# Kernel optimization log

Measured on AMD Instinct MI355X. Metric: run time of the kernel, lower is better.

The kernel has to match this reference:

```python
import jax, jax.numpy as jnp
import numpy as np

N_NODES = 100000
IN_CH = 128
HID = 128   # 2 * out_channels
OUT = 64    # out_channels
N_EDGES = 1000000


def _glorot(key, shape):
    lim = np.sqrt(6.0 / (shape[0] + shape[1]))
    return jax.random.uniform(key, shape, jnp.float32, -lim, lim)


def setup_inputs() -> dict:
    key = jax.random.key(0)
    ks = jax.random.split(key, 8)
    x = jax.random.normal(ks[0], (N_NODES, IN_CH), jnp.float32)
    edge_index = jax.random.randint(ks[1], (2, N_EDGES), 0, N_NODES, jnp.int64)
    return {
        "x": x,
        "edge_index": edge_index,
        # conv1: in -> 2*out
        "W1_l": _glorot(ks[2], (IN_CH, HID)),
        "W1_r": _glorot(ks[3], (IN_CH, HID)),
        "b1": jnp.zeros((HID,), jnp.float32),
        # conv_mu: 2*out -> out
        "Wmu_l": _glorot(ks[4], (HID, OUT)),
        "Wmu_r": _glorot(ks[5], (HID, OUT)),
        "bmu": jnp.zeros((OUT,), jnp.float32),
        # conv_logstd: 2*out -> out
        "Wls_l": _glorot(ks[6], (HID, OUT)),
        "Wls_r": _glorot(ks[7], (HID, OUT)),
        "bls": jnp.zeros((OUT,), jnp.float32),
    }


def _sage_conv(x, src, dst, W_l, W_r, b, n_nodes):
    # mean-aggregate neighbor features: messages flow src -> dst (PyG source_to_target)
    agg = jax.ops.segment_sum(x[src], dst, num_segments=n_nodes)          # [N, d]
    deg = jax.ops.segment_sum(jnp.ones(src.shape, x.dtype), dst, num_segments=n_nodes)
    agg = agg / jnp.maximum(deg, 1.0)[:, None]
    return agg @ W_l + x @ W_r + b


def reference(x, edge_index, W1_l, W1_r, b1, Wmu_l, Wmu_r, bmu, Wls_l, Wls_r, bls):
    src, dst = edge_index[0], edge_index[1]
    n = x.shape[0]
    h = jax.nn.relu(_sage_conv(x, src, dst, W1_l, W1_r, b1, n))
    mu = _sage_conv(h, src, dst, Wmu_l, Wmu_r, bmu, n)
    logstd = _sage_conv(h, src, dst, Wls_l, Wls_r, bls, n)
    return (mu, logstd)
```

## Files before the change

### kernel.cpp

```cpp
#include <hip/hip_runtime.h>

#define NN 100000
#define IC 128
#define OC 64
#define NE 1000000

#define NBUCK 64
#define BN 1568
#define RCAP 18432
#define EPB 2048
#define CAPA 64
#define GPAD 16
#define LDW 136

typedef __attribute__((ext_vector_type(8))) short short8;
typedef __attribute__((ext_vector_type(4))) float f32x4;

static __device__ __forceinline__ float b2f(unsigned short u) {
    unsigned v = ((unsigned)u) << 16;
    float f;
    __builtin_memcpy(&f, &v, 4);
    return f;
}
static __device__ __forceinline__ unsigned short f2b(float f) {
    unsigned u;
    __builtin_memcpy(&u, &f, 4);
    u += 0x7fff + ((u >> 16) & 1);
    return (unsigned short)(u >> 16);
}

__global__ __launch_bounds__(256) void k_binA(const int* __restrict__ src,
                                              const int* __restrict__ dst,
                                              int* __restrict__ gcur,
                                              unsigned* __restrict__ bins) {
    __shared__ unsigned buf[NBUCK][CAPA];
    __shared__ int lcnt[NBUCK];
    const int t = threadIdx.x;
    if (t < NBUCK) lcnt[t] = 0;
    __syncthreads();
    const int e0 = blockIdx.x * EPB;
#pragma unroll
    for (int q = 0; q < EPB / 256; ++q) {
        int e = e0 + q * 256 + t;
        if (e < NE) {
            int d = dst[e];
            int s = src[e];
            int b = d / BN;
            unsigned packed = ((unsigned)(d - b * BN) << 17) | (unsigned)s;
            int idx = atomicAdd(&lcnt[b], 1);
            if (idx < CAPA) {
                buf[b][idx] = packed;
            } else {
                int g = atomicAdd(&gcur[b * GPAD], 1);
                if (g < RCAP) bins[(size_t)b * RCAP + g] = packed;
            }
        }
    }
    __syncthreads();
    const int wid = t >> 6, lane = t & 63;
    for (int b = wid * 16; b < wid * 16 + 16; ++b) {
        int c = lcnt[b];
        if (c > CAPA) c = CAPA;
        if (c > 0) {
            int g = 0;
            if (lane == 0) g = atomicAdd(&gcur[b * GPAD], c);
            g = __shfl(g, 0, 64);
            if (lane < c && g + lane < RCAP)
                bins[(size_t)b * RCAP + g + lane] = buf[b][lane];
        }
    }
}

__global__ __launch_bounds__(64) void k_bscan(const int* __restrict__ gcur,
                                              int* __restrict__ bstart,
                                              int* __restrict__ row_ptr) {
    const int t = threadIdx.x;
    int v = gcur[t * GPAD];
    if (v > RCAP) v = RCAP;
    int s = v;
    for (int off = 1; off < 64; off <<= 1) {
        int u = __shfl_up(s, off, 64);
        if (t >= off) s += u;
    }
    bstart[t] = s - v;
    if (t == 63) row_ptr[NN] = s;
}

__global__ __launch_bounds__(512) void k_binB(const int* __restrict__ gcur,
                                              const int* __restrict__ bstart,
                                              const unsigned* __restrict__ bins,
                                              int* __restrict__ row_ptr,
                                              int* __restrict__ csr) {
    __shared__ int lc[2048];
    __shared__ int rk[2048];
    __shared__ int tsum[512];
    __shared__ int seg[RCAP];
    const int b = blockIdx.x;
    const int t = threadIdx.x;
    const int base = b * BN;
    const int nloc = (NN - base < BN) ? (NN - base) : BN;
    for (int i = t; i < 2048; i += 512) { lc[i] = 0; rk[i] = 0; }
    __syncthreads();
    int c = gcur[b * GPAD];
    if (c > RCAP) c = RCAP;
    const unsigned* mb = bins + (size_t)b * RCAP;
    for (int i = t; i < c; i += 512) atomicAdd(&lc[mb[i] >> 17], 1);
    __syncthreads();
    int loc[4], s = 0;
#pragma unroll
    for (int q = 0; q < 4; ++q) { loc[q] = lc[t * 4 + q]; s += loc[q]; }
    tsum[t] = s;
    __syncthreads();
    for (int off = 1; off < 512; off <<= 1) {
        int u = (t >= off) ? tsum[t - off] : 0;
        __syncthreads();
        tsum[t] += u;
        __syncthreads();
    }
    int run = tsum[t] - s;
#pragma unroll
    for (int q = 0; q < 4; ++q) { lc[t * 4 + q] = run; run += loc[q]; }
    __syncthreads();
    const int bs = bstart[b];
    for (int i = t; i < nloc; i += 512) row_ptr[base + i] = bs + lc[i];
    for (int i = t; i < c; i += 512) {
        unsigned p = mb[i];
        int dl = p >> 17;
        int r = atomicAdd(&rk[dl], 1);
        seg[lc[dl] + r] = (int)(p & 0x1FFFFu);
    }
    __syncthreads();
    for (int i = t; i < c; i += 512) csr[bs + i] = seg[i];
}

__global__ __launch_bounds__(256) void k_cvt(const float* __restrict__ x,
                                             unsigned short* __restrict__ xb) {
    int t = blockIdx.x * 256 + threadIdx.x;
    if (t >= NN * IC / 8) return;
    const float4* p = (const float4*)x + (size_t)t * 2;
    float4 f0 = p[0], f1 = p[1];
    short8 o;
    o[0] = (short)f2b(f0.x); o[1] = (short)f2b(f0.y);
    o[2] = (short)f2b(f0.z); o[3] = (short)f2b(f0.w);
    o[4] = (short)f2b(f1.x); o[5] = (short)f2b(f1.y);
    o[6] = (short)f2b(f1.z); o[7] = (short)f2b(f1.w);
    *((short8*)xb + t) = o;
}

__global__ __launch_bounds__(256) void k_wprep(
    const float* __restrict__ W1l, const float* __restrict__ W1r,
    const float* __restrict__ Wml, const float* __restrict__ Wmr,
    const float* __restrict__ Wsl, const float* __restrict__ Wsr,
    unsigned short* __restrict__ Wf1, unsigned short* __restrict__ Wf2) {
    int t = blockIdx.x * 256 + threadIdx.x;
    if (t >= 2 * 4096) return;
    const int layer = t >> 12;
    const int f = t & 4095;
    const int lane = f & 63;
    const int nt = (f >> 6) & 7;
    const int ks = f >> 9;
    const int col = nt * 16 + (lane & 15);
    const int kb = ks * 32 + ((lane >> 4) << 3);
    short8 o;
#pragma unroll
    for (int e = 0; e < 8; ++e) {
        const int k = kb + e;
        float v;
        if (layer == 0) {
            v = (k < 128) ? W1l[k * 128 + col] : W1r[(k - 128) * 128 + col];
        } else {
            if (col < OC) v = (k < 128) ? Wml[k * OC + col] : Wmr[(k - 128) * OC + col];
            else {
                int c2 = col - OC;
                v = (k < 128) ? Wsl[k * OC + c2] : Wsr[(k - 128) * OC + c2];
            }
        }
        o[e] = (short)f2b(v);
    }
    unsigned short* W = (layer == 0) ? Wf1 : Wf2;
    *(short8*)(W + (size_t)f * 8) = o;
}

__global__ __launch_bounds__(256) void k_agg(const unsigned short* __restrict__ feat,
                                             const int* __restrict__ row_ptr,
                                             const int* __restrict__ csr,
                                             unsigned short* __restrict__ agg) {
    const int lane = threadIdx.x & 63;
    const int wid = threadIdx.x >> 6;
    const int slot = lane >> 4;
    const int cg = lane & 15;
    const int node = blockIdx.x * 16 + wid * 4 + slot;
    if (node >= NN) return;
    const int beg = row_ptr[node];
    const int end = row_ptr[node + 1];
    float acc[8];
#pragma unroll
    for (int q = 0; q < 8; ++q) acc[q] = 0.f;

    for (int j = beg; j < end; j += 8) {
        const int nl = end - j;
        short8 v[8];
#pragma unroll
        for (int u = 0; u < 8; ++u) {
            if (u < nl) {
                int s = csr[j + u];
                v[u] = *(const short8*)(feat + (size_t)s * IC + cg * 8);
            }
        }
#pragma unroll
        for (int u = 0; u < 8; ++u) {
            if (u < nl) {
#pragma unroll
                for (int q = 0; q < 8; ++q) acc[q] += b2f((unsigned short)v[u][q]);
            }
        }
    }
    float inv = 1.0f / fmaxf((float)(end - beg), 1.0f);
    short8 o;
#pragma unroll
    for (int q = 0; q < 8; ++q) o[q] = (short)f2b(acc[q] * inv);
    *(short8*)(agg + (size_t)node * IC + cg * 8) = o;
}

template <int MODE>
__global__ __launch_bounds__(256) void k_gemm(
    const unsigned short* __restrict__ Agg, const unsigned short* __restrict__ Xb,
    const unsigned short* __restrict__ Wf,
    const float* __restrict__ bias0, const float* __restrict__ bias1,
    unsigned short* __restrict__ hout, float* __restrict__ out_mu,
    float* __restrict__ out_ls) {
    const int lane = threadIdx.x & 63;
    const int wid = threadIdx.x >> 6;
    const int rowg = blockIdx.x * 128 + wid * 32;
    const int r16 = lane & 15;
    const int k8 = (lane >> 4) * 8;

    __shared__ short8 bsm[4096];

    int rA[2];
#pragma unroll
    for (int m = 0; m < 2; ++m) {
        int r = rowg + m * 16 + r16;
        rA[m] = (r < NN) ? r : (NN - 1);
    }

    short8 aF[2][8];
#pragma unroll
    for (int ks = 0; ks < 4; ++ks) {
        aF[0][ks] = *(const short8*)(Agg + (size_t)rA[0] * IC + ks * 32 + k8);
        aF[1][ks] = *(const short8*)(Agg + (size_t)rA[1] * IC + ks * 32 + k8);
    }
#pragma unroll
    for (int ks = 0; ks < 4; ++ks) {
        aF[0][4 + ks] = *(const short8*)(Xb + (size_t)rA[0] * IC + ks * 32 + k8);
        aF[1][4 + ks] = *(const short8*)(Xb + (size_t)rA[1] * IC + ks * 32 + k8);
    }

    const short8* Wg = (const short8*)Wf;
#pragma unroll
    for (int i = 0; i < 16; ++i)
        bsm[i * 256 + threadIdx.x] = Wg[i * 256 + threadIdx.x];

#pragma unroll
    for (int ks = 0; ks < 8; ++ks)
        asm volatile("" :: "v"(aF[0][ks]), "v"(aF[1][ks]));

    __syncthreads();

    f32x4 acc[2][8];
#pragma unroll
    for (int m = 0; m < 2; ++m)
#pragma unroll
        for (int nt = 0; nt < 8; ++nt) acc[m][nt] = (f32x4){0.f, 0.f, 0.f, 0.f};

#pragma unroll
    for (int ks = 0; ks < 8; ++ks) {
        short8 bF[8];
#pragma unroll
        for (int nt = 0; nt < 8; ++nt) bF[nt] = bsm[(ks * 8 + nt) * 64 + lane];
#pragma unroll
        for (int nt = 0; nt < 8; ++nt) {
            acc[0][nt] = __builtin_amdgcn_mfma_f32_16x16x32_bf16(aF[0][ks], bF[nt], acc[0][nt], 0, 0, 0);
            acc[1][nt] = __builtin_amdgcn_mfma_f32_16x16x32_bf16(aF[1][ks], bF[nt], acc[1][nt], 0, 0, 0);
        }
    }

    const int rbase = (lane >> 4) * 4;
    if (MODE == 0) {
        __syncthreads();
        unsigned short* ws = (unsigned short*)bsm + wid * 32 * LDW;
#pragma unroll
        for (int m = 0; m < 2; ++m) {
#pragma unroll
            for (int nt = 0; nt < 8; ++nt) {
                const int c = nt * 16 + r16;
                const float bv = bias0[c];
#pragma unroll
                for (int q = 0; q < 4; ++q) {
                    float v = fmaxf(acc[m][nt][q] + bv, 0.f);
                    ws[(m * 16 + rbase + q) * LDW + c] = f2b(v);
                }
            }
        }
        __syncthreads();
#pragma unroll
        for (int p = 0; p < 8; ++p) {
            const int rloc = p * 4 + (lane >> 4);
            const int row = rowg + rloc;
            if (row < NN) {
                short8 v = *(const short8*)&ws[rloc * LDW + r16 * 8];
                *(short8*)(hout + (size_t)row * IC + r16 * 8) = v;
            }
        }
    } else {
#pragma unroll
        for (int m = 0; m < 2; ++m) {
#pragma unroll
            for (int nt = 0; nt < 8; ++nt) {
                const int c = nt * 16 + r16;
                const float bv = (c < OC) ? bias0[c] : bias1[c - OC];
#pragma unroll
                for (int q = 0; q < 4; ++q) {
                    const int row = rowg + m * 16 + rbase + q;
                    if (row >= NN) continue;
                    float v = acc[m][nt][q] + bv;
                    if (c < OC) out_mu[(size_t)row * OC + c] = v;
                    else        out_ls[(size_t)row * OC + (c - OC)] = v;
                }
            }
        }
    }
}

extern "C" void kernel_launch(void* const* d_in, const int* in_sizes, int n_in,
                              void* d_out, int out_size, void* d_ws, size_t ws_size,
                              hipStream_t stream) {
    const float* x   = (const float*)d_in[0];
    const int*   ei  = (const int*)d_in[1];
    const float* W1l = (const float*)d_in[2];
    const float* W1r = (const float*)d_in[3];
    const float* b1  = (const float*)d_in[4];
    const float* Wml = (const float*)d_in[5];
    const float* Wmr = (const float*)d_in[6];
    const float* bm  = (const float*)d_in[7];
    const float* Wsl = (const float*)d_in[8];
    const float* Wsr = (const float*)d_in[9];
    const float* bs  = (const float*)d_in[10];

    const int* src = ei;
    const int* dst = ei + NE;

    char* w = (char*)d_ws;
    unsigned short* xb   = (unsigned short*)(w);
    unsigned short* hb   = (unsigned short*)(w + 25600000);
    unsigned short* aggb = (unsigned short*)(w + 51200000);
    unsigned short* Wf1  = (unsigned short*)(w + 76800000);
    unsigned short* Wf2  = (unsigned short*)(w + 76865536);
    int* row_ptr  = (int*)(w + 76931072);
    int* csr      = (int*)(w + 77331136);
    int* gcur     = (int*)(w + 81331136);
    int* bstart   = (int*)(w + 81335232);
    unsigned* bins = (unsigned*)(w + 81336256);

    float* out_mu = (float*)d_out;
    float* out_ls = out_mu + (size_t)NN * OC;

    const int gemm_grid = (NN + 127) / 128;
    const int agg_grid = (NN + 15) / 16;
    const int binA_grid = (NE + EPB - 1) / EPB;

    hipMemsetAsync(gcur, 0, NBUCK * GPAD * sizeof(int), stream);
    k_binA<<<binA_grid, 256, 0, stream>>>(src, dst, gcur, bins);
    k_bscan<<<1, 64, 0, stream>>>(gcur, bstart, row_ptr);
    k_binB<<<NBUCK, 512, 0, stream>>>(gcur, bstart, bins, row_ptr, csr);

    k_cvt<<<(NN * IC / 8 + 255) / 256, 256, 0, stream>>>(x, xb);
    k_wprep<<<(2 * 4096 + 255) / 256, 256, 0, stream>>>(W1l, W1r, Wml, Wmr, Wsl, Wsr, Wf1, Wf2);

    k_agg<<<agg_grid, 256, 0, stream>>>(xb, row_ptr, csr, aggb);
    k_gemm<0><<<gemm_grid, 256, 0, stream>>>(aggb, xb, Wf1, b1, nullptr,
                                             hb, nullptr, nullptr);

    k_agg<<<agg_grid, 256, 0, stream>>>(hb, row_ptr, csr, aggb);
    k_gemm<1><<<gemm_grid, 256, 0, stream>>>(aggb, hb, Wf2, bm, bs,
                                             nullptr, out_mu, out_ls);
}
```

Before: 200.4 us.

## Fold bucket scan into binB, merge prep kernels, halve GEMM weight LDS

Removes the separate single-block bucket-scan launch by having each binB block recompute the 64-entry prefix scan itself. Merges the x-to-bf16 conversion and weight-packing kernels into one launch. In the GEMM, weights are staged into shared memory in two halves (32 KB instead of 64 KB), with extra barriers between them, to raise occupancy. The cost is an added sync and a second weight load per block in exchange for fewer launches and more resident blocks.

```diff
diff --git a/kernel.cpp b/kernel.cpp
--- a/kernel.cpp
+++ b/kernel.cpp
@@ -12,6 +12,7 @@
 #define CAPA 64
 #define GPAD 16
 #define LDW 136
+#define CVT_BLOCKS 6250
 
 typedef __attribute__((ext_vector_type(8))) short short8;
 typedef __attribute__((ext_vector_type(4))) float f32x4;
@@ -71,23 +72,7 @@
     }
 }
 
-__global__ __launch_bounds__(64) void k_bscan(const int* __restrict__ gcur,
-                                              int* __restrict__ bstart,
-                                              int* __restrict__ row_ptr) {
-    const int t = threadIdx.x;
-    int v = gcur[t * GPAD];
-    if (v > RCAP) v = RCAP;
-    int s = v;
-    for (int off = 1; off < 64; off <<= 1) {
-        int u = __shfl_up(s, off, 64);
-        if (t >= off) s += u;
-    }
-    bstart[t] = s - v;
-    if (t == 63) row_ptr[NN] = s;
-}
-
 __global__ __launch_bounds__(512) void k_binB(const int* __restrict__ gcur,
-                                              const int* __restrict__ bstart,
                                               const unsigned* __restrict__ bins,
                                               int* __restrict__ row_ptr,
                                               int* __restrict__ csr) {
@@ -95,10 +80,22 @@
     __shared__ int rk[2048];
     __shared__ int tsum[512];
     __shared__ int seg[RCAP];
+    __shared__ int sh_bs;
     const int b = blockIdx.x;
     const int t = threadIdx.x;
     const int base = b * BN;
     const int nloc = (NN - base < BN) ? (NN - base) : BN;
+    if (t < 64) {
+        int v = gcur[t * GPAD];
+        if (v > RCAP) v = RCAP;
+        int s = v;
+        for (int off = 1; off < 64; off <<= 1) {
+            int u = __shfl_up(s, off, 64);
+            if (t >= off) s += u;
+        }
+        if (t == b) sh_bs = s - v;
+        if (b == 0 && t == 63) row_ptr[NN] = s;
+    }
     for (int i = t; i < 2048; i += 512) { lc[i] = 0; rk[i] = 0; }
     __syncthreads();
     int c = gcur[b * GPAD];
@@ -121,7 +118,7 @@
 #pragma unroll
     for (int q = 0; q < 4; ++q) { lc[t * 4 + q] = run; run += loc[q]; }
     __syncthreads();
-    const int bs = bstart[b];
+    const int bs = sh_bs;
     for (int i = t; i < nloc; i += 512) row_ptr[base + i] = bs + lc[i];
     for (int i = t; i < c; i += 512) {
         unsigned p = mb[i];
@@ -133,52 +130,52 @@
     for (int i = t; i < c; i += 512) csr[bs + i] = seg[i];
 }
 
-__global__ __launch_bounds__(256) void k_cvt(const float* __restrict__ x,
-                                             unsigned short* __restrict__ xb) {
-    int t = blockIdx.x * 256 + threadIdx.x;
-    if (t >= NN * IC / 8) return;
-    const float4* p = (const float4*)x + (size_t)t * 2;
-    float4 f0 = p[0], f1 = p[1];
-    short8 o;
-    o[0] = (short)f2b(f0.x); o[1] = (short)f2b(f0.y);
-    o[2] = (short)f2b(f0.z); o[3] = (short)f2b(f0.w);
-    o[4] = (short)f2b(f1.x); o[5] = (short)f2b(f1.y);
-    o[6] = (short)f2b(f1.z); o[7] = (short)f2b(f1.w);
-    *((short8*)xb + t) = o;
-}
-
-__global__ __launch_bounds__(256) void k_wprep(
+__global__ __launch_bounds__(256) void k_prep(
+    const float* __restrict__ x, unsigned short* __restrict__ xb,
     const float* __restrict__ W1l, const float* __restrict__ W1r,
     const float* __restrict__ Wml, const float* __restrict__ Wmr,
     const float* __restrict__ Wsl, const float* __restrict__ Wsr,
     unsigned short* __restrict__ Wf1, unsigned short* __restrict__ Wf2) {
-    int t = blockIdx.x * 256 + threadIdx.x;
-    if (t >= 2 * 4096) return;
-    const int layer = t >> 12;
-    const int f = t & 4095;
-    const int lane = f & 63;
-    const int nt = (f >> 6) & 7;
-    const int ks = f >> 9;
-    const int col = nt * 16 + (lane & 15);
-    const int kb = ks * 32 + ((lane >> 4) << 3);
-    short8 o;
-#pragma unroll
-    for (int e = 0; e < 8; ++e) {
-        const int k = kb + e;
-        float v;
-        if (layer == 0) {
-            v = (k < 128) ? W1l[k * 128 + col] : W1r[(k - 128) * 128 + col];
-        } else {
-            if (col < OC) v = (k < 128) ? Wml[k * OC + col] : Wmr[(k - 128) * OC + col];
-            else {
-                int c2 = col - OC;
-                v = (k < 128) ? Wsl[k * OC + c2] : Wsr[(k - 128) * OC + c2];
-            }
-        }
-        o[e] = (short)f2b(v);
-    }
-    unsigned short* W = (layer == 0) ? Wf1 : Wf2;
-    *(short8*)(W + (size_t)f * 8) = o;
+    const int blk = blockIdx.x;
+    if (blk < CVT_BLOCKS) {
+        int t = blk * 256 + threadIdx.x;
+        const float4* p = (const float4*)x + (size_t)t * 2;
+        float4 f0 = p[0], f1 = p[1];
+        short8 o;
+        o[0] = (short)f2b(f0.x); o[1] = (short)f2b(f0.y);
+        o[2] = (short)f2b(f0.z); o[3] = (short)f2b(f0.w);
+        o[4] = (short)f2b(f1.x); o[5] = (short)f2b(f1.y);
+        o[6] = (short)f2b(f1.z); o[7] = (short)f2b(f1.w);
+        *((short8*)xb + t) = o;
+    } else {
+        int t = (blk - CVT_BLOCKS) * 256 + threadIdx.x;
+        if (t >= 2 * 4096) return;
+        const int layer = t >> 12;
+        const int f = t & 4095;
+        const int lane = f & 63;
+        const int nt = (f >> 6) & 7;
+        const int ks = f >> 9;
+        const int col = nt * 16 + (lane & 15);
+        const int kb = ks * 32 + ((lane >> 4) << 3);
+        short8 o;
+#pragma unroll
+        for (int e = 0; e < 8; ++e) {
+            const int k = kb + e;
+            float v;
+            if (layer == 0) {
+                v = (k < 128) ? W1l[k * 128 + col] : W1r[(k - 128) * 128 + col];
+            } else {
+                if (col < OC) v = (k < 128) ? Wml[k * OC + col] : Wmr[(k - 128) * OC + col];
+                else {
+                    int c2 = col - OC;
+                    v = (k < 128) ? Wsl[k * OC + c2] : Wsr[(k - 128) * OC + c2];
+                }
+            }
+            o[e] = (short)f2b(v);
+        }
+        unsigned short* W = (layer == 0) ? Wf1 : Wf2;
+        *(short8*)(W + (size_t)f * 8) = o;
+    }
 }
 
 __global__ __launch_bounds__(256) void k_agg(const unsigned short* __restrict__ feat,
@@ -235,7 +232,8 @@
     const int r16 = lane & 15;
     const int k8 = (lane >> 4) * 8;
 
-    __shared__ short8 bsm[4096];
+    __shared__ unsigned short smem[MODE == 0 ? (4 * 32 * LDW) : 16384];
+    short8* bsm = (short8*)smem;
 
     int rA[2];
 #pragma unroll
@@ -258,7 +256,7 @@
 
     const short8* Wg = (const short8*)Wf;
 #pragma unroll
-    for (int i = 0; i < 16; ++i)
+    for (int i = 0; i < 8; ++i)
         bsm[i * 256 + threadIdx.x] = Wg[i * 256 + threadIdx.x];
 
 #pragma unroll
@@ -274,7 +272,7 @@
         for (int nt = 0; nt < 8; ++nt) acc[m][nt] = (f32x4){0.f, 0.f, 0.f, 0.f};
 
 #pragma unroll
-    for (int ks = 0; ks < 8; ++ks) {
+    for (int ks = 0; ks < 4; ++ks) {
         short8 bF[8];
 #pragma unroll
         for (int nt = 0; nt < 8; ++nt) bF[nt] = bsm[(ks * 8 + nt) * 64 + lane];
@@ -284,11 +282,27 @@
             acc[1][nt] = __builtin_amdgcn_mfma_f32_16x16x32_bf16(aF[1][ks], bF[nt], acc[1][nt], 0, 0, 0);
         }
     }
+    __syncthreads();
+#pragma unroll
+    for (int i = 0; i < 8; ++i)
+        bsm[i * 256 + threadIdx.x] = Wg[2048 + i * 256 + threadIdx.x];
+    __syncthreads();
+#pragma unroll
+    for (int ks = 4; ks < 8; ++ks) {
+        short8 bF[8];
+#pragma unroll
+        for (int nt = 0; nt < 8; ++nt) bF[nt] = bsm[((ks - 4) * 8 + nt) * 64 + lane];
+#pragma unroll
+        for (int nt = 0; nt < 8; ++nt) {
+            acc[0][nt] = __builtin_amdgcn_mfma_f32_16x16x32_bf16(aF[0][ks], bF[nt], acc[0][nt], 0, 0, 0);
+            acc[1][nt] = __builtin_amdgcn_mfma_f32_16x16x32_bf16(aF[1][ks], bF[nt], acc[1][nt], 0, 0, 0);
+        }
+    }
 
     const int rbase = (lane >> 4) * 4;
     if (MODE == 0) {
         __syncthreads();
-        unsigned short* ws = (unsigned short*)bsm + wid * 32 * LDW;
+        unsigned short* ws = smem + wid * 32 * LDW;
 #pragma unroll
         for (int m = 0; m < 2; ++m) {
 #pragma unroll
@@ -359,7 +373,6 @@
     int* row_ptr  = (int*)(w + 76931072);
     int* csr      = (int*)(w + 77331136);
     int* gcur     = (int*)(w + 81331136);
-    int* bstart   = (int*)(w + 81335232);
     unsigned* bins = (unsigned*)(w + 81336256);
 
     float* out_mu = (float*)d_out;
@@ -371,11 +384,9 @@
 
     hipMemsetAsync(gcur, 0, NBUCK * GPAD * sizeof(int), stream);
     k_binA<<<binA_grid, 256, 0, stream>>>(src, dst, gcur, bins);
-    k_bscan<<<1, 64, 0, stream>>>(gcur, bstart, row_ptr);
-    k_binB<<<NBUCK, 512, 0, stream>>>(gcur, bstart, bins, row_ptr, csr);
-
-    k_cvt<<<(NN * IC / 8 + 255) / 256, 256, 0, stream>>>(x, xb);
-    k_wprep<<<(2 * 4096 + 255) / 256, 256, 0, stream>>>(W1l, W1r, Wml, Wmr, Wsl, Wsr, Wf1, Wf2);
+    k_binB<<<NBUCK, 512, 0, stream>>>(gcur, bins, row_ptr, csr);
+
+    k_prep<<<CVT_BLOCKS + 32, 256, 0, stream>>>(x, xb, W1l, W1r, Wml, Wmr, Wsl, Wsr, Wf1, Wf2);
 
     k_agg<<<agg_grid, 256, 0, stream>>>(xb, row_ptr, csr, aggb);
     k_gemm<0><<<gemm_grid, 256, 0, stream>>>(aggb, xb, Wf1, b1, nullptr,
```

New measurement: 198.5 us. Within noise of the previous version (-0.9%).
